# Optimization experiments

Measured on AMD Instinct MI355X. Metric: run time of the kernel, lower is better.

## Reference

```python
import jax, jax.numpy as jnp
import numpy as np

NQ = 8            # data qubits: ceil(log2(256))
NLAYERS = 6       # StronglyEntanglingLayers depth
BATCH = 4096
IN_DIM = 2560
ENC_DIM = 256

def leaky(x):
    return jnp.where(x >= 0, x, 0.2 * x)

def rot_mat(phi, theta, omega):
    # PennyLane Rot(phi,theta,omega) = RZ(omega) @ RY(theta) @ RZ(phi)
    c = jnp.cos(theta / 2); s = jnp.sin(theta / 2)
    m00 = jnp.exp(-0.5j * (phi + omega)) * c
    m01 = -jnp.exp(0.5j * (phi - omega)) * s
    m10 = jnp.exp(-0.5j * (phi - omega)) * s
    m11 = jnp.exp(0.5j * (phi + omega)) * c
    return jnp.stack([jnp.stack([m00, m01]), jnp.stack([m10, m11])])

def apply_1q(psi, U, w):
    psi = jnp.tensordot(U, psi, axes=((1,), (w,)))
    return jnp.moveaxis(psi, 0, w)

def apply_cnot(psi, c, t):
    s = jnp.moveaxis(psi, (c, t), (0, 1))
    s = jnp.stack([s[0], s[1, ::-1]], axis=0)
    return jnp.moveaxis(s, (0, 1), (c, t))

def circuit(amps, params):
    # amps: (256,) complex64 normalized amplitudes; params: (L, NQ, 3)
    psi = amps.reshape((2,) * NQ)
    L = params.shape[0]
    for l in range(L):
        for q in range(NQ):
            psi = apply_1q(psi, rot_mat(params[l, q, 0], params[l, q, 1], params[l, q, 2]), q)
        r = l % (NQ - 1) + 1  # PennyLane default imprimitive ranges
        for q in range(NQ):
            psi = apply_cnot(psi, q, (q + r) % NQ)
    probs = jnp.real(psi * jnp.conj(psi))
    z, xm, ym = [], [], []
    yfac_base = jnp.array([-1j, 1j], dtype=psi.dtype)
    for q in range(NQ):
        axes = tuple(i for i in range(NQ) if i != q)
        p = jnp.sum(probs, axis=axes)
        z.append(p[0] - p[1])
        flipped = jnp.flip(psi, axis=q)
        xm.append(jnp.real(jnp.sum(jnp.conj(psi) * flipped)))
        yfac = yfac_base.reshape([2 if i == q else 1 for i in range(NQ)])
        ym.append(jnp.real(jnp.sum(jnp.conj(psi) * (flipped * yfac))))
    return jnp.stack(z + xm + ym)  # (24,) order: Z..., X..., Y...

def forward(x, ew1, eb1, ew2, eb2, ew3, eb3, dec_params,
            dw1, db1, dw2, db2, dw3, db3, dw4, db4, dw5, db5):
    h = leaky(x @ ew1 + eb1)
    h = leaky(h @ ew2 + eb2)
    enc = jnp.tanh(h @ ew3 + eb3)                      # (B, 256)
    nrm = jnp.linalg.norm(enc, axis=1, keepdims=True)
    amps = jax.lax.stop_gradient(enc / jnp.maximum(nrm, 1e-12)).astype(jnp.complex64)
    meas = jax.vmap(lambda a: circuit(a, dec_params))(amps)  # (B, 24)
    h = leaky(meas @ dw1 + db1)
    h = leaky(h @ dw2 + db2)
    h = leaky(h @ dw3 + db3)
    h = leaky(h @ dw4 + db4)
    return jnp.tanh(h @ dw5 + db5)                     # (B, 2560)

def _lin(key, fin, fout):
    k1, k2 = jax.random.split(key)
    lim = 1.0 / np.sqrt(fin)
    w = jax.random.uniform(k1, (fin, fout), jnp.float32, -lim, lim)
    b = jax.random.uniform(k2, (fout,), jnp.float32, -lim, lim)
    return w, b

def setup_inputs() -> dict:
    key = jax.random.key(0)
    ks = jax.random.split(key, 10)
    x = jax.random.normal(ks[0], (BATCH, IN_DIM), jnp.float32)
    ew1, eb1 = _lin(ks[1], IN_DIM, 1024)
    ew2, eb2 = _lin(ks[2], 1024, 512)
    ew3, eb3 = _lin(ks[3], 512, ENC_DIM)
    dec_params = jax.random.uniform(ks[4], (NLAYERS, NQ, 3), jnp.float32, 0.0, 2 * np.pi)
    dw1, db1 = _lin(ks[5], 3 * NQ, 128)
    dw2, db2 = _lin(ks[6], 128, 256)
    dw3, db3 = _lin(ks[7], 256, 512)
    dw4, db4 = _lin(ks[8], 512, 1024)
    dw5, db5 = _lin(ks[9], 1024, IN_DIM)
    return {"x": x, "ew1": ew1, "eb1": eb1, "ew2": ew2, "eb2": eb2, "ew3": ew3, "eb3": eb3,
            "dec_params": dec_params, "dw1": dw1, "db1": db1, "dw2": dw2, "db2": db2,
            "dw3": dw3, "db3": db3, "dw4": dw4, "db4": db4, "dw5": dw5, "db5": db5}

def reference(x, ew1, eb1, ew2, eb2, ew3, eb3, dec_params,
              dw1, db1, dw2, db2, dw3, db3, dw4, db4, dw5, db5):
    return forward(x, ew1, eb1, ew2, eb2, ew3, eb3, dec_params,
                   dw1, db1, dw2, db2, dw3, db3, dw4, db4, dw5, db5)
```

## Files before the change

kernel.cpp:

```cpp
#include <hip/hip_runtime.h>
#include <hip/hip_bf16.h>


using bf16 = __hip_bfloat16;
typedef __attribute__((ext_vector_type(8))) short short8;
typedef __attribute__((ext_vector_type(4))) short short4v;
typedef __attribute__((ext_vector_type(4))) float f32x4;

template <int V> struct IC { static constexpr int value = V; };

__device__ inline void stf(float* p, size_t i, float v) { p[i] = v; }
__device__ inline void stf(bf16* p, size_t i, float v) { p[i] = __float2bfloat16(v); }

__device__ inline float fast_tanh(float x) {
  x = fminf(fmaxf(x, -15.0f), 15.0f);
  float t = __expf(2.0f * x);
  return __fdividef(t - 1.0f, t + 1.0f);
}

__device__ inline short f2bs(float x) {
  bf16 h = __float2bfloat16(x);
  return *reinterpret_cast<short*>(&h);
}
__device__ inline short8 ld8b(const float* p) {
  const float4 a = ((const float4*)p)[0];
  const float4 b = ((const float4*)p)[1];
  short8 r;
  r[0] = f2bs(a.x); r[1] = f2bs(a.y); r[2] = f2bs(a.z); r[3] = f2bs(a.w);
  r[4] = f2bs(b.x); r[5] = f2bs(b.y); r[6] = f2bs(b.z); r[7] = f2bs(b.w);
  return r;
}
__device__ inline short4v ld4b(const float* p) {
  const float4 a = *(const float4*)p;
  short4v r;
  r[0] = f2bs(a.x); r[1] = f2bs(a.y); r[2] = f2bs(a.z); r[3] = f2bs(a.w);
  return r;
}

__device__ inline void async_load16(const bf16* g, short* l) {
  __builtin_amdgcn_global_load_lds(
      (const __attribute__((address_space(1))) unsigned int*)g,
      (__attribute__((address_space(3))) unsigned int*)l, 16, 0, 0);
}

template <int NC>
__device__ inline void run_circuit_n(float (&re)[NC][4], float (&im)[NC][4],
                                     const float* gsh, int lane) {
  for (int l = 0; l < 6; ++l) {
    for (int qq = 0; qq < 8; ++qq) {
      const float* g = &gsh[(l * 8 + qq) * 8];
      const int s = 1 << (7 - qq);
      if (s >= 4) {
        const int lm = s >> 2;
        const bool hi = (lane & lm) != 0;
        const float g0r = hi ? g[4] : g[0], g0i = hi ? g[5] : g[1];
        const float g1r = hi ? g[6] : g[2], g1i = hi ? g[7] : g[3];
#pragma unroll
        for (int j = 0; j < 4; ++j) {
#pragma unroll
          for (int c = 0; c < NC; ++c) {
            float orr = __shfl_xor(re[c][j], lm, 64);
            float oii = __shfl_xor(im[c][j], lm, 64);
            float p0r = hi ? orr : re[c][j], p0i = hi ? oii : im[c][j];
            float p1r = hi ? re[c][j] : orr, p1i = hi ? im[c][j] : oii;
            re[c][j] = g0r * p0r - g0i * p0i + g1r * p1r - g1i * p1i;
            im[c][j] = g0r * p0i + g0i * p0r + g1r * p1i + g1i * p1r;
          }
        }
      } else {
#pragma unroll
        for (int c = 0; c < NC; ++c) {
#pragma unroll
          for (int j0 = 0; j0 < 4; ++j0) {
            if ((j0 & s) == 0) {
              int j1 = j0 | s;
              float p0r = re[c][j0], p0i = im[c][j0];
              float p1r = re[c][j1], p1i = im[c][j1];
              re[c][j0] = g[0] * p0r - g[1] * p0i + g[2] * p1r - g[3] * p1i;
              im[c][j0] = g[0] * p0i + g[1] * p0r + g[2] * p1i + g[3] * p1r;
              re[c][j1] = g[4] * p0r - g[5] * p0i + g[6] * p1r - g[7] * p1i;
              im[c][j1] = g[4] * p0i + g[5] * p0r + g[6] * p1i + g[7] * p1r;
            }
          }
        }
      }
    }
    const int r = l % 7 + 1;
    for (int qq = 0; qq < 8; ++qq) {
      const int sc = 1 << (7 - qq);
      const int st = 1 << (7 - ((qq + r) & 7));
      if (st >= 4) {
        const int lm = st >> 2;
        if (sc >= 4) {
          const bool ctl = (lane & (sc >> 2)) != 0;
#pragma unroll
          for (int j = 0; j < 4; ++j) {
#pragma unroll
            for (int c = 0; c < NC; ++c) {
              float orr = __shfl_xor(re[c][j], lm, 64);
              float oii = __shfl_xor(im[c][j], lm, 64);
              re[c][j] = ctl ? orr : re[c][j];
              im[c][j] = ctl ? oii : im[c][j];
            }
          }
        } else {
#pragma unroll
          for (int j = 0; j < 4; ++j) {
            if (j & sc) {
#pragma unroll
              for (int c = 0; c < NC; ++c) {
                re[c][j] = __shfl_xor(re[c][j], lm, 64);
                im[c][j] = __shfl_xor(im[c][j], lm, 64);
              }
            }
          }
        }
      } else {
        if (sc >= 4) {
          const bool ctl = (lane & (sc >> 2)) != 0;
#pragma unroll
          for (int c = 0; c < NC; ++c) {
#pragma unroll
            for (int j0 = 0; j0 < 4; ++j0) {
              if ((j0 & st) == 0) {
                int j1 = j0 | st;
                float t0r = re[c][j0], t0i = im[c][j0];
                float t1r = re[c][j1], t1i = im[c][j1];
                re[c][j0] = ctl ? t1r : t0r; im[c][j0] = ctl ? t1i : t0i;
                re[c][j1] = ctl ? t0r : t1r; im[c][j1] = ctl ? t0i : t1i;
              }
            }
          }
        } else {
#pragma unroll
          for (int c = 0; c < NC; ++c) {
#pragma unroll
            for (int j0 = 0; j0 < 4; ++j0) {
              if ((j0 & sc) && (j0 & st) == 0) {
                int j1 = j0 | st;
                float tr = re[c][j0], ti = im[c][j0];
                re[c][j0] = re[c][j1]; im[c][j0] = im[c][j1];
                re[c][j1] = tr; im[c][j1] = ti;
              }
            }
          }
        }
      }
    }
  }
}

__global__ __launch_bounds__(256) void prep_all(
    const float* w0, const float* w1, const float* w2, const float* w3,
    const float* w4, const float* w5, const float* w6, const float* w7,
    const float* b0, const float* b1, const float* b2, const float* b3,
    const float* b4, const float* b5, const float* b6, const float* b7,
    const float* dp, const float* xf,
    bf16* __restrict__ wt, float* __restrict__ biasf, float* __restrict__ gw,
    bf16* __restrict__ xb, bf16* __restrict__ btu, int do_x) {
  int bid = blockIdx.x;
  const int tid = threadIdx.x;

  if (bid < 64) {
    __shared__ float gsh[384];
    if (tid < 48) {
      float phi = dp[tid * 3 + 0], theta = dp[tid * 3 + 1], omega = dp[tid * 3 + 2];
      float c = cosf(0.5f * theta), s = sinf(0.5f * theta);
      float a = 0.5f * (phi + omega), d = 0.5f * (phi - omega);
      float ca = cosf(a), sa = sinf(a), cd = cosf(d), sd = sinf(d);
      float* o = &gsh[tid * 8];
      o[0] =  ca * c; o[1] = -sa * c;
      o[2] = -cd * s; o[3] = -sd * s;
      o[4] =  cd * s; o[5] = -sd * s;
      o[6] =  ca * c; o[7] =  sa * c;
    }
    __syncthreads();
    const int lane = tid & 63;
    const int col = bid * 4 + (tid >> 6);
    float re[1][4], im[1][4];
#pragma unroll
    for (int j = 0; j < 4; ++j) {
      re[0][j] = (lane * 4 + j == col) ? 1.f : 0.f;
      im[0][j] = 0.f;
    }
    run_circuit_n<1>(re, im, gsh, lane);
#pragma unroll
    for (int j = 0; j < 4; ++j) {
      int n = lane * 4 + j;
      {
        bf16 h = __float2bfloat16(re[0][j]);
        float lo = re[0][j] - __bfloat162float(h);
        size_t base = (size_t)n * 768 + col;
        btu[base] = h; btu[base + 256] = h; btu[base + 512] = __float2bfloat16(lo);
      }
      {
        bf16 h = __float2bfloat16(im[0][j]);
        float lo = im[0][j] - __bfloat162float(h);
        size_t base = (size_t)(256 + n) * 768 + col;
        btu[base] = h; btu[base + 256] = h; btu[base + 512] = __float2bfloat16(lo);
      }
    }
    return;
  }
  bid -= 64;

  const int Ks[8]  = {2560, 1024, 512, 24, 128, 256, 512, 1024};
  const int Ns[8]  = {1024, 512, 256, 128, 256, 512, 1024, 2560};
  const int cum[8] = {2560, 3072, 3200, 3204, 3236, 3364, 3876, 6436};
  const long wto[8] = {0, 2621440, 3145728, 3276800, 3280896, 3313664, 3444736, 3969024};
  const float* Wp[8] = {w0, w1, w2, w3, w4, w5, w6, w7};
  const float* Bp[8] = {b0, b1, b2, b3, b4, b5, b6, b7};
  const int boff[8] = {0, 1024, 1536, 1792, 1920, 2176, 2688, 3712};

  if (bid < 805) {
    __shared__ short tile[32][33];
    const int r = tid >> 3, c4 = (tid & 7) << 2;
    const int n = tid >> 3, k4 = (tid & 7) << 2;
    for (int s8 = 0; s8 < 8; ++s8) {
      const int lbid = bid * 8 + s8;
      if (lbid >= 6436) break;
      int t = 0;
      while (lbid >= cum[t]) t++;
      int base = t ? cum[t - 1] : 0;
      int local = lbid - base;
      int K = Ks[t], N = Ns[t];
      int tk = (K + 31) >> 5;
      int kt = local % tk, nt = local / tk;
      int Kp = tk << 5;
      int gk = kt * 32 + r, gn = nt * 32 + c4;
      short4v v;
      if (gk < K) v = ld4b(Wp[t] + (size_t)gk * N + gn);
      else { v[0] = 0; v[1] = 0; v[2] = 0; v[3] = 0; }
      tile[r][c4] = v[0]; tile[r][c4 + 1] = v[1]; tile[r][c4 + 2] = v[2]; tile[r][c4 + 3] = v[3];
      __syncthreads();
      short4v o;
      o[0] = tile[k4][n]; o[1] = tile[k4 + 1][n]; o[2] = tile[k4 + 2][n]; o[3] = tile[k4 + 3][n];
      *(short4v*)&wt[wto[t] + (size_t)(nt * 32 + n) * Kp + kt * 32 + k4] = o;
      __syncthreads();
    }
    return;
  }
  bid -= 805;

  if (bid < 8) {
    int b = bid;
    int nb = Ns[b];
    for (int t2 = tid; t2 < nb; t2 += 256)
      biasf[boff[b] + t2] = Bp[b][t2];
  } else if (bid == 8) {
    int g = tid;
    if (g < 48) {
      float phi = dp[g * 3 + 0], theta = dp[g * 3 + 1], omega = dp[g * 3 + 2];
      float c = cosf(0.5f * theta), s = sinf(0.5f * theta);
      float a = 0.5f * (phi + omega), d = 0.5f * (phi - omega);
      float ca = cosf(a), sa = sinf(a), cd = cosf(d), sd = sinf(d);
      float* o = gw + g * 8;
      o[0] =  ca * c; o[1] = -sa * c;
      o[2] = -cd * s; o[3] = -sd * s;
      o[4] =  cd * s; o[5] = -sd * s;
      o[6] =  ca * c; o[7] =  sa * c;
    }
  } else if (do_x) {
    const int xb8 = bid - 9;
#pragma unroll
    for (int s8 = 0; s8 < 8; ++s8) {
      long i = ((long)(xb8 * 8 + s8) * 256 + tid) * 8;
      if (i < 10485760L) {
        short8 v = ld8b(xf + i);
        *(short8*)((short*)xb + i) = v;
      }
    }
  }
}

template <int BM, int BN, int BK, int WR, int WC, int ACT, typename TC>
__global__ __launch_bounds__(256) void gemm_async(const bf16* __restrict__ A,
                                                  const bf16* __restrict__ Bt,
                                                  const float* __restrict__ bias,
                                                  TC* __restrict__ C,
                                                  int M, int N, int K) {
  constexpr int CPR = BK / 8;
  constexpr int MASK = CPR - 1;
  constexpr int RPW = 64 / CPR;
  constexpr int RPP = 4 * RPW;
  constexpr int WMT = BM / WR;
  constexpr int WNT = BN / WC;
  constexpr int FI = WMT / 16;
  constexpr int FJ = WNT / 16;
  constexpr int KK = BK / 32;
  constexpr int NPA = BM / RPP;
  constexpr int NPB = BN / RPP;
  constexpr int LOADS = NPA + NPB;
  static_assert(LOADS == 4 || LOADS == 6 || LOADS == 8, "vmcnt literal");
  __shared__ __align__(16) short As[2][BM * BK];
  __shared__ __align__(16) short Bs[2][BN * BK];
  const int tid = threadIdx.x;
  const int lane = tid & 63;
  const int wid = tid >> 6;
  const int wm = wid / WC, wn = wid % WC;
  const int bm = blockIdx.y * BM;
  const int bn = blockIdx.x * BN;

  const int st_r = lane / CPR;
  const int st_cs = (lane & MASK) ^ (st_r & MASK);

  const int frag_m = lane & 15;
  const int q = lane >> 4;

  const bf16* pa[NPA];
  const bf16* pb[NPB];
#pragma unroll
  for (int p = 0; p < NPA; ++p)
    pa[p] = A + (size_t)(bm + p * RPP + wid * RPW + st_r) * K + st_cs * 8;
#pragma unroll
  for (int p = 0; p < NPB; ++p)
    pb[p] = Bt + (size_t)(bn + p * RPP + wid * RPW + st_r) * K + st_cs * 8;

  int aoff[FI][KK], boff[FJ][KK];
#pragma unroll
  for (int i = 0; i < FI; ++i) {
    const int m = wm * WMT + i * 16 + frag_m;
#pragma unroll
    for (int kk = 0; kk < KK; ++kk)
      aoff[i][kk] = m * BK + ((((kk * 4 + q) ^ (m & MASK))) << 3);
  }
#pragma unroll
  for (int j = 0; j < FJ; ++j) {
    const int n = wn * WNT + j * 16 + frag_m;
#pragma unroll
    for (int kk = 0; kk < KK; ++kk)
      boff[j][kk] = n * BK + ((((kk * 4 + q) ^ (n & MASK))) << 3);
  }

  auto stage = [&](int buf) {
#pragma unroll
    for (int p = 0; p < NPA; ++p) {
      async_load16(pa[p], &As[buf][(p * RPP + wid * RPW) * BK]);
      pa[p] += BK;
    }
#pragma unroll
    for (int p = 0; p < NPB; ++p) {
      async_load16(pb[p], &Bs[buf][(p * RPP + wid * RPW) * BK]);
      pb[p] += BK;
    }
  };

  f32x4 acc[FI][FJ] = {};

  const int nsteps = K / BK;
  stage(0);
  if (nsteps > 1) stage(1);

  int t = 0;
  const int main_iters = nsteps - 1;

  auto kstep = [&](auto bufc) {
    constexpr int BUF = decltype(bufc)::value;
    if constexpr (LOADS == 8) asm volatile("s_waitcnt vmcnt(8)" ::: "memory");
    else if constexpr (LOADS == 6) asm volatile("s_waitcnt vmcnt(6)" ::: "memory");
    else asm volatile("s_waitcnt vmcnt(4)" ::: "memory");
    __builtin_amdgcn_s_barrier();
    short8 af[FI][KK], bfr[FJ][KK];
#pragma unroll
    for (int i = 0; i < FI; ++i)
#pragma unroll
      for (int kk = 0; kk < KK; ++kk)
        af[i][kk] = *(const short8*)&As[BUF][aoff[i][kk]];
#pragma unroll
    for (int j = 0; j < FJ; ++j)
#pragma unroll
      for (int kk = 0; kk < KK; ++kk)
        bfr[j][kk] = *(const short8*)&Bs[BUF][boff[j][kk]];
    asm volatile("s_waitcnt lgkmcnt(0)" ::: "memory");
    __builtin_amdgcn_sched_barrier(0);
    __builtin_amdgcn_s_barrier();
    if (t + 2 < nsteps) stage(BUF);
#pragma unroll
    for (int kk = 0; kk < KK; ++kk)
#pragma unroll
      for (int i = 0; i < FI; ++i)
#pragma unroll
        for (int j = 0; j < FJ; ++j)
          acc[i][j] = __builtin_amdgcn_mfma_f32_16x16x32_bf16(af[i][kk], bfr[j][kk], acc[i][j], 0, 0, 0);
  };

  while (t + 1 < main_iters) {
    kstep(IC<0>{}); ++t;
    kstep(IC<1>{}); ++t;
  }
  if (t < main_iters) {
    if (t & 1) kstep(IC<1>{});
    else       kstep(IC<0>{});
    ++t;
  }

  asm volatile("s_waitcnt vmcnt(0)" ::: "memory");
  __builtin_amdgcn_s_barrier();
  {
    const short* Ac = As[t & 1];
    const short* Bc = Bs[t & 1];
    short8 af[FI][KK], bfr[FJ][KK];
#pragma unroll
    for (int i = 0; i < FI; ++i)
#pragma unroll
      for (int kk = 0; kk < KK; ++kk)
        af[i][kk] = *(const short8*)&Ac[aoff[i][kk]];
#pragma unroll
    for (int j = 0; j < FJ; ++j)
#pragma unroll
      for (int kk = 0; kk < KK; ++kk)
        bfr[j][kk] = *(const short8*)&Bc[boff[j][kk]];
#pragma unroll
    for (int kk = 0; kk < KK; ++kk)
#pragma unroll
      for (int i = 0; i < FI; ++i)
#pragma unroll
        for (int j = 0; j < FJ; ++j)
          acc[i][j] = __builtin_amdgcn_mfma_f32_16x16x32_bf16(af[i][kk], bfr[j][kk], acc[i][j], 0, 0, 0);
  }

  const int col_lane = lane & 15;
  const int row_quad = q << 2;
#pragma unroll
  for (int i = 0; i < FI; ++i) {
#pragma unroll
    for (int j = 0; j < FJ; ++j) {
      int n = bn + wn * WNT + j * 16 + col_lane;
      float bj = (ACT == 2) ? 0.f : bias[n];
#pragma unroll
      for (int r = 0; r < 4; ++r) {
        int m = bm + wm * WMT + i * 16 + row_quad + r;
        float v = acc[i][j][r] + bj;
        if (ACT == 0) {
          v = (v >= 0.f) ? v : 0.2f * v;
          stf(C, (size_t)m * N + n, v);
        } else if (ACT == 1) {
          stf(C, (size_t)m * N + n, fast_tanh(v));
        } else if (ACT == 2) {
          stf(C, (size_t)m * N + n, v);
        } else {
          float tv = fast_tanh(v);
          bf16 h = __float2bfloat16(tv);
          float lo = tv - __bfloat162float(h);
          size_t base = (size_t)m * 768 + n;
          ((bf16*)C)[base] = h;
          ((bf16*)C)[base + 256] = __float2bfloat16(lo);
          ((bf16*)C)[base + 512] = h;
        }
      }
    }
  }
}

__global__ __launch_bounds__(256) void gemm_cvt(const float* __restrict__ A,
                                                const float* __restrict__ W,
                                                const float* __restrict__ bias,
                                                bf16* __restrict__ C,
                                                int M, int N, int K) {
  __shared__ __align__(16) short As[128 * 40];
  __shared__ __align__(16) short Bs[128 * 40];
  const int tid = threadIdx.x;
  const int lane = tid & 63;
  const int wave = tid >> 6;
  const int wm = wave >> 1, wn = wave & 1;
  const int bm = blockIdx.y * 128;
  const int bn = blockIdx.x * 128;
  const int a_row0 = tid >> 2;
  const int a_kcol = (tid & 3) << 3;
  const int b_ncol = (tid & 31) << 2;
  const int b_krow = (tid >> 5) << 2;
  const int frag_m = lane & 15;
  const int frag_k = (lane >> 4) << 3;

  f32x4 acc[4][4] = {};

  for (int k0 = 0; k0 < K; k0 += 32) {
#pragma unroll
    for (int c = 0; c < 2; ++c) {
      const int row = c * 64 + a_row0;
      short8 v = ld8b(A + (size_t)(bm + row) * K + k0 + a_kcol);
      *(short8*)&As[row * 40 + a_kcol] = v;
    }
    short4v bv[4];
#pragma unroll
    for (int kk = 0; kk < 4; ++kk)
      bv[kk] = ld4b(W + (size_t)(k0 + b_krow + kk) * N + bn + b_ncol);
#pragma unroll
    for (int nn = 0; nn < 4; ++nn) {
      short4v w;
      w[0] = bv[0][nn]; w[1] = bv[1][nn]; w[2] = bv[2][nn]; w[3] = bv[3][nn];
      *(short4v*)&Bs[(b_ncol + nn) * 40 + b_krow] = w;
    }
    __syncthreads();
    short8 af[4], bfr[4];
#pragma unroll
    for (int i = 0; i < 4; ++i)
      af[i] = *(const short8*)&As[(wm * 64 + i * 16 + frag_m) * 40 + frag_k];
#pragma unroll
    for (int j = 0; j < 4; ++j)
      bfr[j] = *(const short8*)&Bs[(wn * 64 + j * 16 + frag_m) * 40 + frag_k];
#pragma unroll
    for (int i = 0; i < 4; ++i)
#pragma unroll
      for (int j = 0; j < 4; ++j)
        acc[i][j] = __builtin_amdgcn_mfma_f32_16x16x32_bf16(af[i], bfr[j], acc[i][j], 0, 0, 0);
    __syncthreads();
  }

  const int col_lane = lane & 15;
  const int row_quad = (lane >> 4) << 2;
#pragma unroll
  for (int i = 0; i < 4; ++i)
#pragma unroll
    for (int j = 0; j < 4; ++j) {
      int n = bn + wn * 64 + j * 16 + col_lane;
      float bj = bias[n];
#pragma unroll
      for (int r = 0; r < 4; ++r) {
        int m = bm + wm * 64 + i * 16 + row_quad + r;
        float v = acc[i][j][r] + bj;
        v = (v >= 0.f) ? v : 0.2f * v;
        stf(C, (size_t)m * N + n, v);
      }
    }
}

__global__ __launch_bounds__(256) void meas_d1(const float* __restrict__ PSI,
                                               const float* __restrict__ dw1,
                                               const float* __restrict__ db1,
                                               bf16* __restrict__ d1out) {
  const int tid = threadIdx.x;
  const int lane = tid & 63;
  const int b = blockIdx.x * 4 + (tid >> 6);

  const float* pp = PSI + (size_t)b * 512;
  float4 ar = *(const float4*)(pp + lane * 4);
  float4 ai = *(const float4*)(pp + 256 + lane * 4);
  float re[4] = {ar.x, ar.y, ar.z, ar.w};
  float im[4] = {ai.x, ai.y, ai.z, ai.w};

  float ss = 0.f;
#pragma unroll
  for (int j = 0; j < 4; ++j) ss += re[j] * re[j] + im[j] * im[j];
#pragma unroll
  for (int o = 32; o; o >>= 1) ss += __shfl_xor(ss, o, 64);
  const float inv = 1.0f / fmaxf(ss, 1e-24f);

  float mz[8], mx[8], my[8];
#pragma unroll
  for (int qq = 0; qq < 8; ++qq) {
    const int s = 1 << (7 - qq);
    float z = 0.f, x = 0.f, y = 0.f;
#pragma unroll
    for (int j = 0; j < 4; ++j) {
      float fr, fi;
      if (s >= 4) {
        fr = __shfl_xor(re[j], s >> 2, 64);
        fi = __shfl_xor(im[j], s >> 2, 64);
      } else {
        fr = re[j ^ s]; fi = im[j ^ s];
      }
      float prob = re[j] * re[j] + im[j] * im[j];
      int i = lane * 4 + j;
      float sg = (i & s) ? -1.f : 1.f;
      z += sg * prob;
      x += re[j] * fr + im[j] * fi;
      y += sg * (re[j] * fi - im[j] * fr);
    }
#pragma unroll
    for (int o = 32; o; o >>= 1) {
      z += __shfl_xor(z, o, 64);
      x += __shfl_xor(x, o, 64);
      y += __shfl_xor(y, o, 64);
    }
    mz[qq] = z * inv; mx[qq] = x * inv; my[qq] = y * inv;
  }

#pragma unroll
  for (int half = 0; half < 2; ++half) {
    const int n = lane + half * 64;
    float acc = db1[n];
#pragma unroll
    for (int qq = 0; qq < 8; ++qq) {
      acc += mz[qq] * dw1[qq * 128 + n];
      acc += mx[qq] * dw1[(8 + qq) * 128 + n];
      acc += my[qq] * dw1[(16 + qq) * 128 + n];
    }
    acc = (acc >= 0.f) ? acc : 0.2f * acc;
    d1out[(size_t)b * 128 + n] = __float2bfloat16(acc);
  }
}

__global__ __launch_bounds__(256) void circuit_wave(const float* __restrict__ enc,
                                                    const float* __restrict__ gw,
                                                    const float* __restrict__ dw1,
                                                    const float* __restrict__ db1,
                                                    bf16* __restrict__ d1out) {
  __shared__ float gsh[384];
  const int tid = threadIdx.x;
  for (int t = tid; t < 384; t += 256) gsh[t] = gw[t];
  __syncthreads();
  const int lane = tid & 63;
  const int b = blockIdx.x * 4 + (tid >> 6);

  float4 e = *(const float4*)(enc + (size_t)b * 256 + lane * 4);
  float re[1][4], im[1][4];
  re[0][0] = e.x; re[0][1] = e.y; re[0][2] = e.z; re[0][3] = e.w;
  im[0][0] = 0.f; im[0][1] = 0.f; im[0][2] = 0.f; im[0][3] = 0.f;
  float ss = e.x * e.x + e.y * e.y + e.z * e.z + e.w * e.w;
#pragma unroll
  for (int o = 32; o; o >>= 1) ss += __shfl_xor(ss, o, 64);
  float inv = 1.0f / fmaxf(sqrtf(ss), 1e-12f);
#pragma unroll
  for (int j = 0; j < 4; ++j) re[0][j] *= inv;

  run_circuit_n<1>(re, im, gsh, lane);

  float mz[8], mx[8], my[8];
#pragma unroll
  for (int qq = 0; qq < 8; ++qq) {
    const int s = 1 << (7 - qq);
    float z = 0.f, x = 0.f, y = 0.f;
#pragma unroll
    for (int j = 0; j < 4; ++j) {
      float fr, fi;
      if (s >= 4) {
        fr = __shfl_xor(re[0][j], s >> 2, 64);
        fi = __shfl_xor(im[0][j], s >> 2, 64);
      } else {
        fr = re[0][j ^ s]; fi = im[0][j ^ s];
      }
      float prob = re[0][j] * re[0][j] + im[0][j] * im[0][j];
      int i = lane * 4 + j;
      float sg = (i & s) ? -1.f : 1.f;
      z += sg * prob;
      x += re[0][j] * fr + im[0][j] * fi;
      y += sg * (re[0][j] * fi - im[0][j] * fr);
    }
#pragma unroll
    for (int o = 32; o; o >>= 1) {
      z += __shfl_xor(z, o, 64);
      x += __shfl_xor(x, o, 64);
      y += __shfl_xor(y, o, 64);
    }
    mz[qq] = z; mx[qq] = x; my[qq] = y;
  }

#pragma unroll
  for (int half = 0; half < 2; ++half) {
    const int n = lane + half * 64;
    float acc = db1[n];
#pragma unroll
    for (int qq = 0; qq < 8; ++qq) {
      acc += mz[qq] * dw1[qq * 128 + n];
      acc += mx[qq] * dw1[(8 + qq) * 128 + n];
      acc += my[qq] * dw1[(16 + qq) * 128 + n];
    }
    acc = (acc >= 0.f) ? acc : 0.2f * acc;
    d1out[(size_t)b * 128 + n] = __float2bfloat16(acc);
  }
}

extern "C" void kernel_launch(void* const* d_in, const int* in_sizes, int n_in,
                              void* d_out, int out_size, void* d_ws, size_t ws_size,
                              hipStream_t stream) {
  (void)in_sizes; (void)n_in; (void)out_size;
  char* wsb = (char*)d_ws;
  float* gw    = (float*)(wsb + 256);
  float* biasf = (float*)(wsb + 4096);
  float* encf  = (float*)(wsb + 294912);
  bf16*  BtU   = (bf16*)(wsb + 294912);
  bf16*  P     = (bf16*)(wsb + 4489216);
  bf16*  Q     = (bf16*)(wsb + 12877824);
  bf16*  WT    = (bf16*)(wsb + 17072128);
  bf16*  Xb    = (bf16*)(wsb + 30253056);
  bf16*  Ap    = (bf16*)(wsb + 30253056);
  float* PSI   = (float*)(wsb + 36544512);
  const bool have_xb = ws_size >= 51224576;

  bf16* ew1t = WT + 0;
  bf16* ew2t = WT + 2621440;
  bf16* ew3t = WT + 3145728;
  bf16* dw2t = WT + 3280896;
  bf16* dw3t = WT + 3313664;
  bf16* dw4t = WT + 3444736;
  bf16* dw5t = WT + 3969024;
  float* beb1 = biasf + 0;
  float* beb2 = biasf + 1024;
  float* beb3 = biasf + 1536;
  float* bdb2 = biasf + 1920;
  float* bdb3 = biasf + 2176;
  float* bdb4 = biasf + 2688;
  float* bdb5 = biasf + 3712;

  prep_all<<<1518, 256, 0, stream>>>(
      (const float*)d_in[1], (const float*)d_in[3], (const float*)d_in[5],
      (const float*)d_in[8], (const float*)d_in[10], (const float*)d_in[12],
      (const float*)d_in[14], (const float*)d_in[16],
      (const float*)d_in[2], (const float*)d_in[4], (const float*)d_in[6],
      (const float*)d_in[9], (const float*)d_in[11], (const float*)d_in[13],
      (const float*)d_in[15], (const float*)d_in[17],
      (const float*)d_in[7], (const float*)d_in[0],
      WT, biasf, gw, Xb, BtU, have_xb ? 1 : 0);

  if (have_xb) {
    gemm_async<64, 64, 64, 2, 2, 0, bf16><<<dim3(16, 64), 256, 0, stream>>>(
        Xb, ew1t, beb1, P, 4096, 1024, 2560);
  } else {
    gemm_cvt<<<dim3(8, 32), 256, 0, stream>>>(
        (const float*)d_in[0], (const float*)d_in[1], beb1, P, 4096, 1024, 2560);
  }

  gemm_async<64, 64, 64, 2, 2, 0, bf16><<<dim3(8, 64), 256, 0, stream>>>(
      P, ew2t, beb2, Q, 4096, 512, 1024);

  if (have_xb) {
    gemm_async<64, 64, 64, 2, 2, 3, bf16><<<dim3(4, 64), 256, 0, stream>>>(
        Q, ew3t, beb3, Ap, 4096, 256, 512);
    gemm_async<64, 64, 64, 2, 2, 2, float><<<dim3(8, 64), 256, 0, stream>>>(
        Ap, BtU, beb3 , PSI, 4096, 512, 768);
    meas_d1<<<1024, 256, 0, stream>>>(PSI, (const float*)d_in[8],
                                      (const float*)d_in[9], Q);
  } else {
    gemm_async<64, 64, 64, 2, 2, 1, float><<<dim3(4, 64), 256, 0, stream>>>(
        Q, ew3t, beb3, encf, 4096, 256, 512);
    circuit_wave<<<1024, 256, 0, stream>>>(encf, gw, (const float*)d_in[8],
                                           (const float*)d_in[9], Q);
  }

  gemm_async<64, 64, 64, 2, 2, 0, bf16><<<dim3(4, 64), 256, 0, stream>>>(
      Q, dw2t, bdb2, P, 4096, 256, 128);
  gemm_async<64, 64, 64, 2, 2, 0, bf16><<<dim3(8, 64), 256, 0, stream>>>(
      P, dw3t, bdb3, Q, 4096, 512, 256);
  gemm_async<64, 64, 64, 2, 2, 0, bf16><<<dim3(16, 64), 256, 0, stream>>>(
      Q, dw4t, bdb4, P, 4096, 1024, 512);
  gemm_async<64, 64, 64, 2, 2, 1, float><<<dim3(40, 64), 256, 0, stream>>>(
      P, dw5t, bdb5, (float*)d_out, 4096, 2560, 1024);
}
```

Before: 281.3 us.

## Load B fragments directly from global into registers, bypassing shared memory

The GEMM kernel no longer stages the B (weight) tile through LDS. Each wave loads its MFMA B fragments straight from global memory into a double-buffered register array, one k-step ahead, while A still uses async LDS staging. This removes B's LDS traffic and halves shared memory use, which may raise occupancy. In exchange it adds redundant global loads across waves that share the same B columns, plus extra register pressure, and the vmcnt wait counts now assume a specific ordering of the interleaved loads.

```diff
diff --git a/kernel.cpp b/kernel.cpp
--- a/kernel.cpp
+++ b/kernel.cpp
@@ -289,11 +289,8 @@
   constexpr int FJ = WNT / 16;
   constexpr int KK = BK / 32;
   constexpr int NPA = BM / RPP;
-  constexpr int NPB = BN / RPP;
-  constexpr int LOADS = NPA + NPB;
-  static_assert(LOADS == 4 || LOADS == 6 || LOADS == 8, "vmcnt literal");
+  static_assert(NPA == 2 || NPA == 4, "vmcnt literal");
   __shared__ __align__(16) short As[2][BM * BK];
-  __shared__ __align__(16) short Bs[2][BN * BK];
   const int tid = threadIdx.x;
   const int lane = tid & 63;
   const int wid = tid >> 6;
@@ -308,15 +305,18 @@
   const int q = lane >> 4;
 
   const bf16* pa[NPA];
-  const bf16* pb[NPB];
 #pragma unroll
   for (int p = 0; p < NPA; ++p)
     pa[p] = A + (size_t)(bm + p * RPP + wid * RPW + st_r) * K + st_cs * 8;
-#pragma unroll
-  for (int p = 0; p < NPB; ++p)
-    pb[p] = Bt + (size_t)(bn + p * RPP + wid * RPW + st_r) * K + st_cs * 8;
-
-  int aoff[FI][KK], boff[FJ][KK];
+
+  const bf16* pbf[FJ][KK];
+#pragma unroll
+  for (int j = 0; j < FJ; ++j)
+#pragma unroll
+    for (int kk = 0; kk < KK; ++kk)
+      pbf[j][kk] = Bt + (size_t)(bn + wn * WNT + j * 16 + frag_m) * K + q * 8 + kk * 32;
+
+  int aoff[FI][KK];
 #pragma unroll
   for (int i = 0; i < FI; ++i) {
     const int m = wm * WMT + i * 16 + frag_m;
@@ -324,64 +324,64 @@
     for (int kk = 0; kk < KK; ++kk)
       aoff[i][kk] = m * BK + ((((kk * 4 + q) ^ (m & MASK))) << 3);
   }
-#pragma unroll
-  for (int j = 0; j < FJ; ++j) {
-    const int n = wn * WNT + j * 16 + frag_m;
-#pragma unroll
-    for (int kk = 0; kk < KK; ++kk)
-      boff[j][kk] = n * BK + ((((kk * 4 + q) ^ (n & MASK))) << 3);
-  }
-
-  auto stage = [&](int buf) {
+
+  auto stageA = [&](int buf) {
 #pragma unroll
     for (int p = 0; p < NPA; ++p) {
       async_load16(pa[p], &As[buf][(p * RPP + wid * RPW) * BK]);
       pa[p] += BK;
     }
-#pragma unroll
-    for (int p = 0; p < NPB; ++p) {
-      async_load16(pb[p], &Bs[buf][(p * RPP + wid * RPW) * BK]);
-      pb[p] += BK;
-    }
   };
 
+  short8 bfr[2][FJ][KK];
+  auto loadB = [&](auto pc) {
+    constexpr int PB = decltype(pc)::value;
+#pragma unroll
+    for (int j = 0; j < FJ; ++j)
+#pragma unroll
+      for (int kk = 0; kk < KK; ++kk) {
+        bfr[PB][j][kk] = *(const short8*)pbf[j][kk];
+        pbf[j][kk] += BK;
+      }
+  };
+
   f32x4 acc[FI][FJ] = {};
 
   const int nsteps = K / BK;
-  stage(0);
-  if (nsteps > 1) stage(1);
+  stageA(0);
+  __builtin_amdgcn_sched_barrier(0);
+  loadB(IC<0>{});
+  __builtin_amdgcn_sched_barrier(0);
+  if (nsteps > 1) stageA(1);
 
   int t = 0;
   const int main_iters = nsteps - 1;
 
   auto kstep = [&](auto bufc) {
     constexpr int BUF = decltype(bufc)::value;
-    if constexpr (LOADS == 8) asm volatile("s_waitcnt vmcnt(8)" ::: "memory");
-    else if constexpr (LOADS == 6) asm volatile("s_waitcnt vmcnt(6)" ::: "memory");
-    else asm volatile("s_waitcnt vmcnt(4)" ::: "memory");
+    if constexpr (NPA == 4) asm volatile("s_waitcnt vmcnt(4)" ::: "memory");
+    else asm volatile("s_waitcnt vmcnt(2)" ::: "memory");
     __builtin_amdgcn_s_barrier();
-    short8 af[FI][KK], bfr[FJ][KK];
+    short8 af[FI][KK];
 #pragma unroll
     for (int i = 0; i < FI; ++i)
 #pragma unroll
       for (int kk = 0; kk < KK; ++kk)
         af[i][kk] = *(const short8*)&As[BUF][aoff[i][kk]];
-#pragma unroll
-    for (int j = 0; j < FJ; ++j)
-#pragma unroll
-      for (int kk = 0; kk < KK; ++kk)
-        bfr[j][kk] = *(const short8*)&Bs[BUF][boff[j][kk]];
     asm volatile("s_waitcnt lgkmcnt(0)" ::: "memory");
     __builtin_amdgcn_sched_barrier(0);
     __builtin_amdgcn_s_barrier();
-    if (t + 2 < nsteps) stage(BUF);
+    if (t + 1 < nsteps) loadB(IC<BUF ^ 1>{});
+    __builtin_amdgcn_sched_barrier(0);
+    if (t + 2 < nsteps) stageA(BUF);
+    __builtin_amdgcn_sched_barrier(0);
 #pragma unroll
     for (int kk = 0; kk < KK; ++kk)
 #pragma unroll
       for (int i = 0; i < FI; ++i)
 #pragma unroll
         for (int j = 0; j < FJ; ++j)
-          acc[i][j] = __builtin_amdgcn_mfma_f32_16x16x32_bf16(af[i][kk], bfr[j][kk], acc[i][j], 0, 0, 0);
+          acc[i][j] = __builtin_amdgcn_mfma_f32_16x16x32_bf16(af[i][kk], bfr[BUF][j][kk], acc[i][j], 0, 0, 0);
   };
 
   while (t + 1 < main_iters) {
@@ -396,28 +396,24 @@
 
   asm volatile("s_waitcnt vmcnt(0)" ::: "memory");
   __builtin_amdgcn_s_barrier();
-  {
-    const short* Ac = As[t & 1];
-    const short* Bc = Bs[t & 1];
-    short8 af[FI][KK], bfr[FJ][KK];
+  auto fin = [&](auto bufc) {
+    constexpr int BUF = decltype(bufc)::value;
+    short8 af[FI][KK];
 #pragma unroll
     for (int i = 0; i < FI; ++i)
 #pragma unroll
       for (int kk = 0; kk < KK; ++kk)
-        af[i][kk] = *(const short8*)&Ac[aoff[i][kk]];
-#pragma unroll
-    for (int j = 0; j < FJ; ++j)
-#pragma unroll
-      for (int kk = 0; kk < KK; ++kk)
-        bfr[j][kk] = *(const short8*)&Bc[boff[j][kk]];
+        af[i][kk] = *(const short8*)&As[BUF][aoff[i][kk]];
 #pragma unroll
     for (int kk = 0; kk < KK; ++kk)
 #pragma unroll
       for (int i = 0; i < FI; ++i)
 #pragma unroll
         for (int j = 0; j < FJ; ++j)
-          acc[i][j] = __builtin_amdgcn_mfma_f32_16x16x32_bf16(af[i][kk], bfr[j][kk], acc[i][j], 0, 0, 0);
-  }
+          acc[i][j] = __builtin_amdgcn_mfma_f32_16x16x32_bf16(af[i][kk], bfr[BUF][j][kk], acc[i][j], 0, 0, 0);
+  };
+  if ((nsteps - 1) & 1) fin(IC<1>{});
+  else                  fin(IC<0>{});
 
   const int col_lane = lane & 15;
   const int row_quad = q << 2;
```

New measurement: 409.7 us. +45.6%, slower.

## Deepen GEMM async LDS pipeline from double to triple buffering

Applied to the files above, without the earlier changes.

The async-load GEMM now keeps three LDS stages in flight instead of two, prefetching two k-steps ahead and waiting with vmcnt(8) in steady state. The loop is reorganized into a three-way rotation with explicit drain steps using vmcnt(4) and vmcnt(0). The goal is to hide more global memory latency behind MFMA work. In exchange it uses 50% more shared memory per block, which may lower occupancy, and it restricts the kernel to 64x64 tile configurations.

```diff
diff --git a/kernel.cpp b/kernel.cpp
--- a/kernel.cpp
+++ b/kernel.cpp
@@ -291,9 +291,9 @@
   constexpr int NPA = BM / RPP;
   constexpr int NPB = BN / RPP;
   constexpr int LOADS = NPA + NPB;
-  static_assert(LOADS == 4 || LOADS == 6 || LOADS == 8, "vmcnt literal");
-  __shared__ __align__(16) short As[2][BM * BK];
-  __shared__ __align__(16) short Bs[2][BN * BK];
+  static_assert(LOADS == 4, "vmcnt literals assume 64x64 tiles");
+  __shared__ __align__(16) short As[3][BM * BK];
+  __shared__ __align__(16) short Bs[3][BN * BK];
   const int tid = threadIdx.x;
   const int lane = tid & 63;
   const int wid = tid >> 6;
@@ -348,17 +348,18 @@
   f32x4 acc[FI][FJ] = {};
 
   const int nsteps = K / BK;
+  int t = 0;
+
   stage(0);
   if (nsteps > 1) stage(1);
-
-  int t = 0;
-  const int main_iters = nsteps - 1;
-
-  auto kstep = [&](auto bufc) {
+  if (nsteps > 2) stage(2);
+
+  auto kstep = [&](auto bufc, auto wc) {
     constexpr int BUF = decltype(bufc)::value;
-    if constexpr (LOADS == 8) asm volatile("s_waitcnt vmcnt(8)" ::: "memory");
-    else if constexpr (LOADS == 6) asm volatile("s_waitcnt vmcnt(6)" ::: "memory");
-    else asm volatile("s_waitcnt vmcnt(4)" ::: "memory");
+    constexpr int WCNT = decltype(wc)::value;
+    if constexpr (WCNT == 8) asm volatile("s_waitcnt vmcnt(8)" ::: "memory");
+    else if constexpr (WCNT == 4) asm volatile("s_waitcnt vmcnt(4)" ::: "memory");
+    else asm volatile("s_waitcnt vmcnt(0)" ::: "memory");
     __builtin_amdgcn_s_barrier();
     short8 af[FI][KK], bfr[FJ][KK];
 #pragma unroll
@@ -374,7 +375,7 @@
     asm volatile("s_waitcnt lgkmcnt(0)" ::: "memory");
     __builtin_amdgcn_sched_barrier(0);
     __builtin_amdgcn_s_barrier();
-    if (t + 2 < nsteps) stage(BUF);
+    if (t + 3 < nsteps) stage(BUF);
 #pragma unroll
     for (int kk = 0; kk < KK; ++kk)
 #pragma unroll
@@ -384,39 +385,30 @@
           acc[i][j] = __builtin_amdgcn_mfma_f32_16x16x32_bf16(af[i][kk], bfr[j][kk], acc[i][j], 0, 0, 0);
   };
 
-  while (t + 1 < main_iters) {
-    kstep(IC<0>{}); ++t;
-    kstep(IC<1>{}); ++t;
-  }
-  if (t < main_iters) {
-    if (t & 1) kstep(IC<1>{});
-    else       kstep(IC<0>{});
+  const int steady = nsteps - 2;
+  while (t + 2 < steady) {
+    kstep(IC<0>{}, IC<8>{}); ++t;
+    kstep(IC<1>{}, IC<8>{}); ++t;
+    kstep(IC<2>{}, IC<8>{}); ++t;
+  }
+  while (t < steady) {
+    switch (t % 3) {
+      case 0: kstep(IC<0>{}, IC<8>{}); break;
+      case 1: kstep(IC<1>{}, IC<8>{}); break;
+      default: kstep(IC<2>{}, IC<8>{}); break;
+    }
     ++t;
   }
-
-  asm volatile("s_waitcnt vmcnt(0)" ::: "memory");
-  __builtin_amdgcn_s_barrier();
-  {
-    const short* Ac = As[t & 1];
-    const short* Bc = Bs[t & 1];
-    short8 af[FI][KK], bfr[FJ][KK];
-#pragma unroll
-    for (int i = 0; i < FI; ++i)
-#pragma unroll
-      for (int kk = 0; kk < KK; ++kk)
-        af[i][kk] = *(const short8*)&Ac[aoff[i][kk]];
-#pragma unroll
-    for (int j = 0; j < FJ; ++j)
-#pragma unroll
-      for (int kk = 0; kk < KK; ++kk)
-        bfr[j][kk] = *(const short8*)&Bc[boff[j][kk]];
-#pragma unroll
-    for (int kk = 0; kk < KK; ++kk)
-#pragma unroll
-      for (int i = 0; i < FI; ++i)
-#pragma unroll
-        for (int j = 0; j < FJ; ++j)
-          acc[i][j] = __builtin_amdgcn_mfma_f32_16x16x32_bf16(af[i][kk], bfr[j][kk], acc[i][j], 0, 0, 0);
+  switch (t % 3) {
+    case 0: kstep(IC<0>{}, IC<4>{}); break;
+    case 1: kstep(IC<1>{}, IC<4>{}); break;
+    default: kstep(IC<2>{}, IC<4>{}); break;
+  }
+  ++t;
+  switch (t % 3) {
+    case 0: kstep(IC<0>{}, IC<0>{}); break;
+    case 1: kstep(IC<1>{}, IC<0>{}); break;
+    default: kstep(IC<2>{}, IC<0>{}); break;
   }
 
   const int col_lane = lane & 15;
```

After: 293.2 us. 1.04x slower.
